# Performance work log

Hardware: AMD Instinct MI355X
Metric: run time of the kernel (lower is better)

## Reference

```python
import jax, jax.numpy as jnp
import numpy as np

N_NODES = 50000
N_EDGES = 800000
IN_DIM = 256
OUT_DIM = 64
HEADS = 4
NEG_SLOPE = 0.2  # PyG GATConv default


def setup_inputs() -> dict:
    key = jax.random.key(0)
    k1, k2, k3, k4, k5, k6 = jax.random.split(key, 6)
    x = jax.random.normal(k1, (N_NODES, IN_DIM), dtype=jnp.float32)
    edge_index = jax.random.randint(k2, (2, N_EDGES), 0, N_NODES, dtype=jnp.int64)
    scale = 1.0 / np.sqrt(IN_DIM)
    W = jax.random.normal(k3, (IN_DIM, HEADS * OUT_DIM), dtype=jnp.float32) * scale
    att_src = jax.random.normal(k4, (HEADS, OUT_DIM), dtype=jnp.float32) * scale
    att_dst = jax.random.normal(k5, (HEADS, OUT_DIM), dtype=jnp.float32) * scale
    bias = jnp.zeros((HEADS * OUT_DIM,), dtype=jnp.float32)
    return {"x": x, "edge_index": edge_index, "W": W,
            "att_src": att_src, "att_dst": att_dst, "bias": bias}


def reference(x, edge_index, W, att_src, att_dst, bias):
    N = x.shape[0]
    H, C = att_src.shape
    # add self loops (PyG GATConv default add_self_loops=True)
    loop = jnp.arange(N, dtype=edge_index.dtype)
    src = jnp.concatenate([edge_index[0], loop])  # [E+N] source j
    dst = jnp.concatenate([edge_index[1], loop])  # [E+N] target i
    # linear projection, per-head features  [N, H, C]
    h = (x @ W).reshape(N, H, C)
    # attention logits: a_src . h_j + a_dst . h_i  -> [E, H]
    a_src = jnp.einsum('nhc,hc->nh', h, att_src)
    a_dst = jnp.einsum('nhc,hc->nh', h, att_dst)
    e = jax.nn.leaky_relu(a_src[src] + a_dst[dst], negative_slope=NEG_SLOPE)
    # edge softmax over incoming edges of each destination node
    m = jax.ops.segment_max(e, dst, num_segments=N)          # [N, H]
    p = jnp.exp(e - m[dst])                                  # [E, H]
    denom = jax.ops.segment_sum(p, dst, num_segments=N)      # [N, H]
    alpha = p / (denom[dst] + 1e-16)                         # [E, H]
    # weighted scatter-aggregate of gathered source features
    out = jax.ops.segment_sum(alpha[:, :, None] * h[src], dst, num_segments=N)
    out = out.reshape(N, H * C) + bias
    return jax.nn.relu(out)  # GATLayer active_func
```

## Files before the change

### kernel.cpp

```cpp
#include <hip/hip_runtime.h>

constexpr int N  = 50000;
constexpr int E  = 800000;
constexpr int K  = 256;
constexpr int F  = 256;
constexpr int H  = 4;
constexpr float SLOPE = 0.2f;

constexpr int CAPS = 6;

constexpr int WT_ROWS = 272;

constexpr size_t OFF_HB   = 0;
constexpr size_t OFF_WT   = OFF_HB   + (size_t)N * F * 2;
constexpr size_t OFF_ASRC = OFF_WT   + (size_t)WT_ROWS * K * 2;
constexpr size_t OFF_ADST = OFF_ASRC + (size_t)N * H * 4;
constexpr size_t OFF_DEG  = OFF_ADST + (size_t)N * H * 4;
constexpr size_t OFF_FLAG = OFF_DEG  + (size_t)N * 4;
constexpr size_t OFF_CSR  = OFF_FLAG + 64;

constexpr int HIST_BLOCKS = 128;
constexpr int GEMM_TILES  = (N + 127) / 128;
constexpr int GEMM_BLOCKS = GEMM_TILES * 2;

typedef short short8 __attribute__((ext_vector_type(8)));
typedef float floatx4 __attribute__((ext_vector_type(4)));

__device__ __forceinline__ float leaky(float x) {
    return x > 0.f ? x : SLOPE * x;
}
__device__ __forceinline__ float blo(unsigned u) { return __uint_as_float(u << 16); }
__device__ __forceinline__ float bhi(unsigned u) { return __uint_as_float(u & 0xffff0000u); }
__device__ __forceinline__ unsigned short f2b(float f) {
    unsigned u = __float_as_uint(f);
    return (unsigned short)((u + 0x7fffu + ((u >> 16) & 1u)) >> 16);
}
__device__ __forceinline__ unsigned pk2(float a, float b) {
    return (unsigned)f2b(a) | ((unsigned)f2b(b) << 16);
}

__device__ __forceinline__ int edge_at(const void* ei, int is64, size_t i) {
    if (is64) return (int)((const long long*)ei)[i];
    return ((const int*)ei)[i];
}

__global__ __launch_bounds__(256)
void prep(const float* __restrict__ Wm, const float* __restrict__ att_src,
          const float* __restrict__ att_dst, const unsigned* __restrict__ ei_words,
          unsigned short* __restrict__ Wt, int* __restrict__ flag,
          int4* __restrict__ zero_region) {
    __shared__ float tile[64][65];
    const int bid = blockIdx.x;
    const int t = threadIdx.x;
    if (bid < 16) {
        const int k0 = (bid & 3) * 64;
        const int n0 = (bid >> 2) * 64;
        const int r = t >> 2;
        const int c4 = (t & 3) * 16;
        #pragma unroll
        for (int i = 0; i < 16; i += 4) {
            float4 v = *reinterpret_cast<const float4*>(
                Wm + (size_t)(k0 + r) * F + n0 + c4 + i);
            tile[r][c4 + i + 0] = v.x;
            tile[r][c4 + i + 1] = v.y;
            tile[r][c4 + i + 2] = v.z;
            tile[r][c4 + i + 3] = v.w;
        }
        __syncthreads();
        unsigned pk[8];
        #pragma unroll
        for (int j = 0; j < 8; ++j)
            pk[j] = pk2(tile[c4 + 2 * j + 0][r], tile[c4 + 2 * j + 1][r]);
        unsigned short* dst = Wt + (size_t)(n0 + r) * K + k0 + c4;
        *reinterpret_cast<uint4*>(dst)     = make_uint4(pk[0], pk[1], pk[2], pk[3]);
        *reinterpret_cast<uint4*>(dst + 8) = make_uint4(pk[4], pk[5], pk[6], pk[7]);
    } else if (bid == 16) {
        const int k = t;
        #pragma unroll
        for (int h = 0; h < H; ++h) {
            const float* wr = Wm + (size_t)k * F + h * 64;
            float s = 0.f, d = 0.f;
            #pragma unroll 8
            for (int c = 0; c < 64; ++c) {
                float w = wr[c];
                s += w * att_src[h * 64 + c];
                d += w * att_dst[h * 64 + c];
            }
            Wt[(size_t)(256 + h) * K + k] = f2b(s);
            Wt[(size_t)(260 + h) * K + k] = f2b(d);
        }
        #pragma unroll
        for (int r = 0; r < 8; ++r) Wt[(size_t)(264 + r) * K + k] = 0;
    } else if (bid == 17) {
        if (t < 64) {
            unsigned v = ei_words[2 * t + 1];
            unsigned long long b = __ballot(v != 0u);
            if (t == 0) *flag = (b == 0ull) ? 1 : 0;
        }
    } else {
        int idx = (bid - 18) * 256 + t;
        if (idx < 12500) zero_region[idx] = make_int4(0, 0, 0, 0);
    }
}

constexpr int LDA = 72;
constexpr int LDW = 72;

__global__ __launch_bounds__(512, 4)
void gemm_hist(const float* __restrict__ X, const unsigned short* __restrict__ Wt,
               unsigned short* __restrict__ Hb, float* __restrict__ asrc,
               float* __restrict__ adst, const void* __restrict__ ei,
               const int* __restrict__ flag, int* __restrict__ deg,
               int* __restrict__ csr) {
    __shared__ unsigned short Al[128 * LDA];
    __shared__ unsigned short Wl[144 * LDW];
    const int tid = threadIdx.x;

    if (blockIdx.x < HIST_BLOCKS) {
        const int is64 = *flag;
        for (int i = blockIdx.x * 512 + tid; i < E; i += HIST_BLOCKS * 512) {
            int d = edge_at(ei, is64, (size_t)E + i);
            int s = edge_at(ei, is64, (size_t)i);
            int r = atomicAdd(&deg[d], 1);
            csr[(d << CAPS) + r] = s;
        }
        return;
    }

    const int bid = blockIdx.x - HIST_BLOCKS;
    const int tileR = bid >> 1;
    const int halfC = bid & 1;
    const int m0 = tileR * 128;
    const int c0 = halfC * 128;

    const int wv = tid >> 6, lane = tid & 63;
    const int quad = lane >> 4, l15 = lane & 15;
    const int rH = wv >> 2;
    const int cQ = wv & 3;
    const bool fusedw = (halfC == 1) && (cQ == 3);

    floatx4 acc[4][2];
    #pragma unroll
    for (int i = 0; i < 4; ++i)
        #pragma unroll
        for (int j = 0; j < 2; ++j) acc[i][j] = (floatx4)0.f;
    floatx4 accf[4];
    #pragma unroll
    for (int i = 0; i < 4; ++i) accf[i] = (floatx4)0.f;

    const int ar = tid >> 2;
    const int akc = (tid & 3) * 16;
    const bool arow_ok = (m0 + ar) < N;
    const int wr = tid >> 2;
    const int wkc = (tid & 3) * 16;

    for (int k0 = 0; k0 < K; k0 += 64) {
        {
            const float* src = X + (size_t)(m0 + ar) * K + k0 + akc;
            unsigned short* dst = &Al[ar * LDA + akc];
            #pragma unroll
            for (int i = 0; i < 16; i += 4) {
                float4 v = arow_ok ? *reinterpret_cast<const float4*>(src + i)
                                   : make_float4(0.f, 0.f, 0.f, 0.f);
                *reinterpret_cast<uint2*>(dst + i) =
                    make_uint2(pk2(v.x, v.y), pk2(v.z, v.w));
            }
        }
        {
            const unsigned short* src = Wt + (size_t)(c0 + wr) * K + k0 + wkc;
            unsigned short* dst = &Wl[wr * LDW + wkc];
            *reinterpret_cast<int4*>(dst)     = *reinterpret_cast<const int4*>(src);
            *reinterpret_cast<int4*>(dst + 8) = *reinterpret_cast<const int4*>(src + 8);
        }
        if (halfC == 1 && tid < 64) {
            const int fr = tid >> 2;
            const int fk = (tid & 3) * 16;
            const unsigned short* src = Wt + (size_t)(256 + fr) * K + k0 + fk;
            unsigned short* dst = &Wl[(128 + fr) * LDW + fk];
            *reinterpret_cast<int4*>(dst)     = *reinterpret_cast<const int4*>(src);
            *reinterpret_cast<int4*>(dst + 8) = *reinterpret_cast<const int4*>(src + 8);
        }
        __syncthreads();
        #pragma unroll
        for (int kk = 0; kk < 64; kk += 32) {
            short8 a[4];
            #pragma unroll
            for (int i = 0; i < 4; ++i)
                a[i] = *reinterpret_cast<const short8*>(
                    &Al[(rH * 64 + i * 16 + l15) * LDA + kk + quad * 8]);
            #pragma unroll
            for (int j = 0; j < 2; ++j) {
                short8 b = *reinterpret_cast<const short8*>(
                    &Wl[(cQ * 32 + j * 16 + l15) * LDW + kk + quad * 8]);
                #pragma unroll
                for (int i = 0; i < 4; ++i)
                    acc[i][j] = __builtin_amdgcn_mfma_f32_16x16x32_bf16(
                        a[i], b, acc[i][j], 0, 0, 0);
            }
            if (fusedw) {
                short8 bf = *reinterpret_cast<const short8*>(
                    &Wl[(128 + l15) * LDW + kk + quad * 8]);
                #pragma unroll
                for (int i = 0; i < 4; ++i)
                    accf[i] = __builtin_amdgcn_mfma_f32_16x16x32_bf16(
                        a[i], bf, accf[i], 0, 0, 0);
            }
        }
        __syncthreads();
    }
    #pragma unroll
    for (int i = 0; i < 4; ++i) {
        const int rbase = m0 + rH * 64 + i * 16 + quad * 4;
        #pragma unroll
        for (int j = 0; j < 2; ++j) {
            const int col = c0 + cQ * 32 + j * 16 + l15;
            #pragma unroll
            for (int r = 0; r < 4; ++r) {
                int row = rbase + r;
                if (row < N) Hb[(size_t)row * F + col] = f2b(acc[i][j][r]);
            }
        }
    }
    if (fusedw) {
        #pragma unroll
        for (int i = 0; i < 4; ++i) {
            const int rbase = m0 + rH * 64 + i * 16 + quad * 4;
            #pragma unroll
            for (int r = 0; r < 4; ++r) {
                int row = rbase + r;
                if (row < N) {
                    if (l15 < 4)      asrc[row * H + l15] = accf[i][r];
                    else if (l15 < 8) adst[row * H + (l15 - 4)] = accf[i][r];
                }
            }
        }
    }
}

__global__ __launch_bounds__(256, 8)
void aggregate(const unsigned short* __restrict__ Hb, const float* __restrict__ asrc,
               const float* __restrict__ adst, const int* __restrict__ deg,
               const int* __restrict__ csr, const float* __restrict__ bias,
               float* __restrict__ out) {
    const int wv = threadIdx.x >> 6;
    const int lane = threadIdx.x & 63;
    const int half = lane >> 5;
    const int l32 = lane & 31;
    const int hd = l32 >> 3;
    const int node = blockIdx.x * 4 + wv;

    const char* hbase = (const char*)Hb;
    const char* abase = (const char*)asrc;
    const unsigned lsh = (unsigned)l32 << 4;
    const unsigned hsh = (unsigned)hd << 2;

    const float adsti = adst[node * H + hd];
    const int start = node << CAPS;
    const int end = start + deg[node];

    float denom = 0.f;
    float a0 = 0.f, a1 = 0.f, a2 = 0.f, a3 = 0.f;
    float a4 = 0.f, a5 = 0.f, a6 = 0.f, a7 = 0.f;
    int e = start;
    for (; e + 8 <= end; e += 8) {
        unsigned s[4]; float l[4]; uint4 u[4];
        #pragma unroll
        for (int j = 0; j < 4; ++j) s[j] = (unsigned)csr[e + 2 * j + half];
        #pragma unroll
        for (int j = 0; j < 4; ++j)
            l[j] = *(const float*)(abase + ((s[j] << 4) + hsh));
        #pragma unroll
        for (int j = 0; j < 4; ++j)
            u[j] = *(const uint4*)(hbase + ((s[j] << 9) + lsh));
        #pragma unroll
        for (int j = 0; j < 4; ++j) {
            float p = __expf(leaky(l[j] + adsti));
            denom += p;
            a0 += p * blo(u[j].x); a1 += p * bhi(u[j].x);
            a2 += p * blo(u[j].y); a3 += p * bhi(u[j].y);
            a4 += p * blo(u[j].z); a5 += p * bhi(u[j].z);
            a6 += p * blo(u[j].w); a7 += p * bhi(u[j].w);
        }
    }
    for (; e + 2 <= end; e += 2) {
        unsigned s0 = (unsigned)csr[e + half];
        float l0 = *(const float*)(abase + ((s0 << 4) + hsh));
        uint4 u0 = *(const uint4*)(hbase + ((s0 << 9) + lsh));
        float p = __expf(leaky(l0 + adsti));
        denom += p;
        a0 += p * blo(u0.x); a1 += p * bhi(u0.x);
        a2 += p * blo(u0.y); a3 += p * bhi(u0.y);
        a4 += p * blo(u0.z); a5 += p * bhi(u0.z);
        a6 += p * blo(u0.w); a7 += p * bhi(u0.w);
    }
    {
        const int rem = end - e;
        bool active;
        unsigned sf;
        if (half == 0) { active = (rem == 1); sf = active ? (unsigned)csr[e] : 0u; }
        else           { active = true;       sf = (unsigned)node; }
        if (active) {
            float l0 = *(const float*)(abase + ((sf << 4) + hsh));
            uint4 u0 = *(const uint4*)(hbase + ((sf << 9) + lsh));
            float p = __expf(leaky(l0 + adsti));
            denom += p;
            a0 += p * blo(u0.x); a1 += p * bhi(u0.x);
            a2 += p * blo(u0.y); a3 += p * bhi(u0.y);
            a4 += p * blo(u0.z); a5 += p * bhi(u0.z);
            a6 += p * blo(u0.w); a7 += p * bhi(u0.w);
        }
    }
    a0 += __shfl_xor(a0, 32); a1 += __shfl_xor(a1, 32);
    a2 += __shfl_xor(a2, 32); a3 += __shfl_xor(a3, 32);
    a4 += __shfl_xor(a4, 32); a5 += __shfl_xor(a5, 32);
    a6 += __shfl_xor(a6, 32); a7 += __shfl_xor(a7, 32);
    denom += __shfl_xor(denom, 32);
    if (half == 0) {
        const float inv = 1.f / (denom + 1e-16f);
        float4 b0 = *reinterpret_cast<const float4*>(bias + l32 * 8);
        float4 b1 = *reinterpret_cast<const float4*>(bias + l32 * 8 + 4);
        float4 o0, o1;
        o0.x = fmaxf(a0 * inv + b0.x, 0.f);
        o0.y = fmaxf(a1 * inv + b0.y, 0.f);
        o0.z = fmaxf(a2 * inv + b0.z, 0.f);
        o0.w = fmaxf(a3 * inv + b0.w, 0.f);
        o1.x = fmaxf(a4 * inv + b1.x, 0.f);
        o1.y = fmaxf(a5 * inv + b1.y, 0.f);
        o1.z = fmaxf(a6 * inv + b1.z, 0.f);
        o1.w = fmaxf(a7 * inv + b1.w, 0.f);
        float* orow = out + (size_t)node * F + l32 * 8;
        *reinterpret_cast<float4*>(orow)     = o0;
        *reinterpret_cast<float4*>(orow + 4) = o1;
    }
}

extern "C" void kernel_launch(void* const* d_in, const int* in_sizes, int n_in,
                              void* d_out, int out_size, void* d_ws, size_t ws_size,
                              hipStream_t stream) {
    const float* x       = (const float*)d_in[0];
    const void*  ei      = d_in[1];
    const float* Wm      = (const float*)d_in[2];
    const float* att_src = (const float*)d_in[3];
    const float* att_dst = (const float*)d_in[4];
    const float* bias    = (const float*)d_in[5];
    float* out = (float*)d_out;

    char* ws = (char*)d_ws;
    unsigned short* hb = (unsigned short*)(ws + OFF_HB);
    unsigned short* wt = (unsigned short*)(ws + OFF_WT);
    float* asrc = (float*)(ws + OFF_ASRC);
    float* adst = (float*)(ws + OFF_ADST);
    int* deg  = (int*)(ws + OFF_DEG);
    int* flag = (int*)(ws + OFF_FLAG);
    int* csr  = (int*)(ws + OFF_CSR);

    prep<<<67, 256, 0, stream>>>(Wm, att_src, att_dst, (const unsigned*)ei,
                                 wt, flag, (int4*)(ws + OFF_DEG));
    gemm_hist<<<HIST_BLOCKS + GEMM_BLOCKS, 512, 0, stream>>>(
        x, wt, hb, asrc, adst, ei, flag, deg, csr);
    aggregate<<<N / 4, 256, 0, stream>>>(hb, asrc, adst, deg, csr, bias, out);
}
```

Measured before the change: 231.6 us.

## Shrink GEMM tiles to 64 rows, unroll histogram loop, pack bf16 stores

Switches the fused GEMM/histogram kernel from 512-thread blocks with 128-row tiles to 256-thread blocks with 64-row tiles, which doubles the GEMM block count and the histogram block count. The edge histogram loop now issues four independent loads and atomics per iteration to raise memory-level parallelism. The GEMM epilogue uses lane shuffles to pack four bf16 values into one 8-byte store instead of scattered 2-byte stores. Smaller tiles give better load balance across CUs but reload the W tile more often, adding extra global traffic.

```diff
diff --git a/kernel.cpp b/kernel.cpp
--- a/kernel.cpp
+++ b/kernel.cpp
@@ -19,8 +19,8 @@
 constexpr size_t OFF_FLAG = OFF_DEG  + (size_t)N * 4;
 constexpr size_t OFF_CSR  = OFF_FLAG + 64;
 
-constexpr int HIST_BLOCKS = 128;
-constexpr int GEMM_TILES  = (N + 127) / 128;
+constexpr int HIST_BLOCKS = 256;
+constexpr int GEMM_TILES  = (N + 63) / 64;
 constexpr int GEMM_BLOCKS = GEMM_TILES * 2;
 
 typedef short short8 __attribute__((ext_vector_type(8)));
@@ -106,19 +106,39 @@
 constexpr int LDA = 72;
 constexpr int LDW = 72;
 
-__global__ __launch_bounds__(512, 4)
+__global__ __launch_bounds__(256, 5)
 void gemm_hist(const float* __restrict__ X, const unsigned short* __restrict__ Wt,
                unsigned short* __restrict__ Hb, float* __restrict__ asrc,
                float* __restrict__ adst, const void* __restrict__ ei,
                const int* __restrict__ flag, int* __restrict__ deg,
                int* __restrict__ csr) {
-    __shared__ unsigned short Al[128 * LDA];
+    __shared__ unsigned short Al[64 * LDA];
     __shared__ unsigned short Wl[144 * LDW];
     const int tid = threadIdx.x;
 
     if (blockIdx.x < HIST_BLOCKS) {
         const int is64 = *flag;
-        for (int i = blockIdx.x * 512 + tid; i < E; i += HIST_BLOCKS * 512) {
+        const int stride = HIST_BLOCKS * 256;
+        int i = blockIdx.x * 256 + tid;
+        for (; i + 3 * stride < E; i += 4 * stride) {
+            int d0 = edge_at(ei, is64, (size_t)E + i);
+            int d1 = edge_at(ei, is64, (size_t)E + i + stride);
+            int d2 = edge_at(ei, is64, (size_t)E + i + 2 * stride);
+            int d3 = edge_at(ei, is64, (size_t)E + i + 3 * stride);
+            int s0 = edge_at(ei, is64, (size_t)i);
+            int s1 = edge_at(ei, is64, (size_t)i + stride);
+            int s2 = edge_at(ei, is64, (size_t)i + 2 * stride);
+            int s3 = edge_at(ei, is64, (size_t)i + 3 * stride);
+            int r0 = atomicAdd(&deg[d0], 1);
+            int r1 = atomicAdd(&deg[d1], 1);
+            int r2 = atomicAdd(&deg[d2], 1);
+            int r3 = atomicAdd(&deg[d3], 1);
+            csr[(d0 << CAPS) + r0] = s0;
+            csr[(d1 << CAPS) + r1] = s1;
+            csr[(d2 << CAPS) + r2] = s2;
+            csr[(d3 << CAPS) + r3] = s3;
+        }
+        for (; i < E; i += stride) {
             int d = edge_at(ei, is64, (size_t)E + i);
             int s = edge_at(ei, is64, (size_t)i);
             int r = atomicAdd(&deg[d], 1);
@@ -130,14 +150,12 @@
     const int bid = blockIdx.x - HIST_BLOCKS;
     const int tileR = bid >> 1;
     const int halfC = bid & 1;
-    const int m0 = tileR * 128;
+    const int m0 = tileR * 64;
     const int c0 = halfC * 128;
 
     const int wv = tid >> 6, lane = tid & 63;
     const int quad = lane >> 4, l15 = lane & 15;
-    const int rH = wv >> 2;
-    const int cQ = wv & 3;
-    const bool fusedw = (halfC == 1) && (cQ == 3);
+    const bool fusedw = (halfC == 1) && (wv == 3);
 
     floatx4 acc[4][2];
     #pragma unroll
@@ -151,8 +169,8 @@
     const int ar = tid >> 2;
     const int akc = (tid & 3) * 16;
     const bool arow_ok = (m0 + ar) < N;
-    const int wr = tid >> 2;
-    const int wkc = (tid & 3) * 16;
+    const int wr = tid >> 1;
+    const int wkc = (tid & 1) * 32;
 
     for (int k0 = 0; k0 < K; k0 += 64) {
         {
@@ -169,8 +187,10 @@
         {
             const unsigned short* src = Wt + (size_t)(c0 + wr) * K + k0 + wkc;
             unsigned short* dst = &Wl[wr * LDW + wkc];
-            *reinterpret_cast<int4*>(dst)     = *reinterpret_cast<const int4*>(src);
-            *reinterpret_cast<int4*>(dst + 8) = *reinterpret_cast<const int4*>(src + 8);
+            #pragma unroll
+            for (int i = 0; i < 32; i += 8)
+                *reinterpret_cast<int4*>(dst + i) =
+                    *reinterpret_cast<const int4*>(src + i);
         }
         if (halfC == 1 && tid < 64) {
             const int fr = tid >> 2;
@@ -187,11 +207,11 @@
             #pragma unroll
             for (int i = 0; i < 4; ++i)
                 a[i] = *reinterpret_cast<const short8*>(
-                    &Al[(rH * 64 + i * 16 + l15) * LDA + kk + quad * 8]);
+                    &Al[(i * 16 + l15) * LDA + kk + quad * 8]);
             #pragma unroll
             for (int j = 0; j < 2; ++j) {
                 short8 b = *reinterpret_cast<const short8*>(
-                    &Wl[(cQ * 32 + j * 16 + l15) * LDW + kk + quad * 8]);
+                    &Wl[(wv * 32 + j * 16 + l15) * LDW + kk + quad * 8]);
                 #pragma unroll
                 for (int i = 0; i < 4; ++i)
                     acc[i][j] = __builtin_amdgcn_mfma_f32_16x16x32_bf16(
@@ -210,21 +230,28 @@
     }
     #pragma unroll
     for (int i = 0; i < 4; ++i) {
-        const int rbase = m0 + rH * 64 + i * 16 + quad * 4;
+        const int row = m0 + i * 16 + quad * 4;
         #pragma unroll
         for (int j = 0; j < 2; ++j) {
-            const int col = c0 + cQ * 32 + j * 16 + l15;
+            const int colb = c0 + wv * 32 + j * 16;
             #pragma unroll
             for (int r = 0; r < 4; ++r) {
-                int row = rbase + r;
-                if (row < N) Hb[(size_t)row * F + col] = f2b(acc[i][j][r]);
+                float v = acc[i][j][r];
+                float vn = __shfl_xor(v, 1);
+                unsigned p = pk2(v, vn);
+                unsigned q = __shfl_xor(p, 2);
+                if ((l15 & 3) == 0 && (row + r) < N) {
+                    *reinterpret_cast<uint2*>(
+                        &Hb[(size_t)(row + r) * F + colb + l15]) =
+                        make_uint2(p, q);
+                }
             }
         }
     }
     if (fusedw) {
         #pragma unroll
         for (int i = 0; i < 4; ++i) {
-            const int rbase = m0 + rH * 64 + i * 16 + quad * 4;
+            const int rbase = m0 + i * 16 + quad * 4;
             #pragma unroll
             for (int r = 0; r < 4; ++r) {
                 int row = rbase + r;
@@ -356,7 +383,7 @@
 
     prep<<<67, 256, 0, stream>>>(Wm, att_src, att_dst, (const unsigned*)ei,
                                  wt, flag, (int4*)(ws + OFF_DEG));
-    gemm_hist<<<HIST_BLOCKS + GEMM_BLOCKS, 512, 0, stream>>>(
+    gemm_hist<<<HIST_BLOCKS + GEMM_BLOCKS, 256, 0, stream>>>(
         x, wt, hb, asrc, adst, ei, flag, deg, csr);
     aggregate<<<N / 4, 256, 0, stream>>>(hb, asrc, adst, deg, csr, bias, out);
 }
```

New measurement: 245.8 us. +6.1%, slower.
